# Optimization experiments

Measured on AMD Instinct MI355X. Metric: run time of the kernel, lower is better.

## Reference

```python
import jax, jax.numpy as jnp
import numpy as np

MAX_DEPTH = 83.0
PI = 3.1415926535
SCALE = 8
FOCAL = 715.0

def setup_inputs() -> dict:
    key = jax.random.key(0)
    ks = jax.random.split(key, 16)
    B, C, H, W = 16, 128, 44, 152
    x = jax.random.normal(ks[0], (B, C, H, W), dtype=jnp.float32)
    # reduction 1x1 convs: 128->64->32->16->8->4
    chans = [128, 64, 32, 16, 8, 4]
    inp = {"x": x}
    for i in range(5):
        cin, cout = chans[i], chans[i + 1]
        w = jax.random.normal(ks[1 + 2 * i], (cout, cin), dtype=jnp.float32) * (1.0 / np.sqrt(cin))
        b = jax.random.normal(ks[2 + 2 * i], (cout,), dtype=jnp.float32) * 0.01
        inp[f"w{i}"] = w
        inp[f"b{i}"] = b
    # final 1x1 conv: 4 -> 3
    inp["cw"] = jax.random.normal(ks[11], (3, 4), dtype=jnp.float32) * 0.5
    inp["cb"] = jax.random.normal(ks[12], (3,), dtype=jnp.float32) * 0.01
    return inp

def _lpg_block(x, w0, b0, w1, b1, w2, b2, w3, b3, w4, b4, cw, cb):
    # reduction chain: 1x1 conv + ELU
    for w, b in ((w0, b0), (w1, b1), (w2, b2), (w3, b3), (w4, b4)):
        x = jax.nn.elu(jnp.einsum('oc,bchw->bohw', w, x) + b[None, :, None, None])
    # 4 -> 3 conv producing (theta, phi, dist) logits
    y = jnp.einsum('oc,bchw->bohw', cw, x) + cb[None, :, None, None]
    theta = jax.nn.sigmoid(y[:, 0]) * PI / 6.0          # [B,H,W]
    phi = jax.nn.sigmoid(y[:, 1]) * PI * 2.0
    dist = jax.nn.sigmoid(y[:, 2]) * MAX_DEPTH
    n1 = jnp.sin(theta) * jnp.cos(phi)
    n2 = jnp.sin(theta) * jnp.sin(phi)
    n3 = jnp.cos(theta)
    n = jnp.stack([n1, n2, n3], axis=1)                  # [B,3,H,W]
    # F.normalize(p=2, dim=1, eps=1e-12)
    norm = jnp.sqrt(jnp.sum(n * n, axis=1, keepdims=True))
    n = n / jnp.maximum(norm, 1e-12)
    n1, n2, n3 = n[:, 0], n[:, 1], n[:, 2]
    # LPG expansion: depth[b, y*s+ii, x*s+jj] = dist / (n1*u[jj] + n2*v[ii] + n3)
    s = SCALE
    off = (jnp.arange(s, dtype=jnp.float32) - (s - 1) / 2.0) / s / FOCAL  # [s]
    v = off[:, None]   # rows (ii)
    u = off[None, :]   # cols (jj)
    denom = (n1[..., None, None] * u + n2[..., None, None] * v
             + n3[..., None, None])                       # [B,H,W,s,s]
    depth = dist[..., None, None] / denom                 # [B,H,W,s,s]
    B, H, W = dist.shape
    depth = jnp.transpose(depth, (0, 1, 3, 2, 4)).reshape(B, 1, H * s, W * s)
    return depth

def reference(x, w0, b0, w1, b1, w2, b2, w3, b3, w4, b4, cw, cb):
    return _lpg_block(x, w0, b0, w1, b1, w2, b2, w3, b3, w4, b4, cw, cb)
```

## Files before the change

kernel.cpp:

```cpp
#include <hip/hip_runtime.h>
#include <math.h>

#define HW_   6688
#define W_    152
#define NPIX  107008
#define OW_   1216
#define OHW_  428032

typedef _Float16 f16;
typedef _Float16 f16x2 __attribute__((ext_vector_type(2)));
typedef _Float16 f16x4 __attribute__((ext_vector_type(4)));
typedef _Float16 f16x8 __attribute__((ext_vector_type(8)));
typedef float    f32x4 __attribute__((ext_vector_type(4)));

#define MFMA(a,b,c) __builtin_amdgcn_mfma_f32_16x16x32_f16((a),(b),(c),0,0,0)

#define SX_STR   136
#define SA1_STR  40
#define SA2_OFF  5120
#define SA2_STR  24
#define SA3_OFF  8192
#define SA3_STR  16
#define SA0_OFFB 34816
#define SA0_STR  72
#define LDSB     53248

__device__ __forceinline__ float fast_sigmoid(float v) {
    return __builtin_amdgcn_rcpf(1.0f + __expf(-v));
}
__device__ __forceinline__ float eluf(float v) {
    return v > 0.0f ? v : (__expf(v) - 1.0f);
}
__device__ __forceinline__ void split8(const float* v, f16x8& hi, f16x8& lo) {
#pragma unroll
    for (int e = 0; e < 8; ++e) {
        f16 h = (f16)v[e];
        hi[e] = h;
        lo[e] = (f16)(v[e] - (float)h);
    }
}
__device__ __forceinline__ f16x4 elu_cvt4(f32x4 a) {
    f16x4 r;
    r[0] = (f16)eluf(a[0]); r[1] = (f16)eluf(a[1]);
    r[2] = (f16)eluf(a[2]); r[3] = (f16)eluf(a[3]);
    return r;
}

__global__ __launch_bounds__(256)
void lpg_mfma(const float* __restrict__ x,
              const float* __restrict__ w0, const float* __restrict__ b0,
              const float* __restrict__ w1, const float* __restrict__ b1,
              const float* __restrict__ w2, const float* __restrict__ b2,
              const float* __restrict__ w3, const float* __restrict__ b3,
              const float* __restrict__ w4, const float* __restrict__ b4,
              const float* __restrict__ cw, const float* __restrict__ cb,
              float* __restrict__ out) {
    __shared__ __align__(16) unsigned char S[LDSB];
    f16* SX  = (f16*)S;
    f16* SA0 = (f16*)(S + SA0_OFFB);

    const int tid  = threadIdx.x;
    const int wv   = __builtin_amdgcn_readfirstlane(tid >> 6);
    const int lane = tid & 63;
    const int p    = lane & 15;
    const int q    = lane >> 4;
    const int pixbase = blockIdx.x * 128;

    {
        const int i     = tid & 127;
        const int chalf = (tid >> 7) * 64;
        int pix = pixbase + i;
        int bb  = pix / HW_;
        int hw  = pix - bb * HW_;
        const float* xp = x + ((size_t)bb * 128 + chalf) * HW_ + hw;
        f16* dst = SX + i * SX_STR + chalf;
#pragma unroll 8
        for (int k = 0; k < 32; ++k) {
            float v0 = xp[(size_t)(2 * k) * HW_];
            float v1 = xp[(size_t)(2 * k + 1) * HW_];
            f16x2 h; h[0] = (f16)v0; h[1] = (f16)v1;
            *(f16x2*)(dst + 2 * k) = h;
        }
    }

    f16x8 w0h[4], w0l[4];
    {
        const float* wr = w0 + (wv * 16 + p) * 128 + q * 8;
#pragma unroll
        for (int kt = 0; kt < 4; ++kt) {
            float v[8];
#pragma unroll
            for (int e = 0; e < 8; ++e) v[e] = wr[kt * 32 + e];
            split8(v, w0h[kt], w0l[kt]);
        }
    }
    f16x8 w1h[2][2], w1l[2][2];
#pragma unroll
    for (int Mt = 0; Mt < 2; ++Mt)
#pragma unroll
        for (int kt = 0; kt < 2; ++kt) {
            float v[8];
#pragma unroll
            for (int e = 0; e < 8; ++e) v[e] = w1[(Mt * 16 + p) * 64 + kt * 32 + q * 8 + e];
            split8(v, w1h[Mt][kt], w1l[Mt][kt]);
        }
    f16x8 w2h, w2l;
    {
        float v[8];
#pragma unroll
        for (int e = 0; e < 8; ++e) v[e] = w2[p * 32 + q * 8 + e];
        split8(v, w2h, w2l);
    }
    f16x8 w3h, w3l;
    {
        float v[8];
        bool ok = (p < 8) && (q < 2);
#pragma unroll
        for (int e = 0; e < 8; ++e) v[e] = ok ? w3[p * 16 + q * 8 + e] : 0.0f;
        split8(v, w3h, w3l);
    }
    f16x8 w4h, w4l;
    {
        float v[8];
        bool ok = (p < 4) && (q == 0);
#pragma unroll
        for (int e = 0; e < 8; ++e) v[e] = ok ? w4[p * 8 + e] : 0.0f;
        split8(v, w4h, w4l);
    }
    f16x8 whh, whl;
    {
        float v[8];
        bool ok = (p < 3) && (q == 0);
#pragma unroll
        for (int e = 0; e < 8; ++e) v[e] = (ok && e < 4) ? cw[p * 4 + e] : 0.0f;
        split8(v, whh, whl);
    }

    const f32x4 z4 = {0.f, 0.f, 0.f, 0.f};
    f32x4 b0v  = *(const f32x4*)(b0 + wv * 16 + 4 * q);
    f32x4 b1v0 = *(const f32x4*)(b1 + 4 * q);
    f32x4 b1v1 = *(const f32x4*)(b1 + 16 + 4 * q);
    f32x4 b2v  = *(const f32x4*)(b2 + 4 * q);
    f32x4 b3v  = *(const f32x4*)(b3 + (q & 1) * 4);
    f32x4 b4v  = *(const f32x4*)(b4);
    float cb0v = cb[0], cb1v = cb[1], cb2v = cb[2];

    __syncthreads();

#pragma unroll 2
    for (int t = 0; t < 8; ++t) {
        const f16* bp = SX + (t * 16 + p) * SX_STR + q * 8;
        f32x4 acc = b0v;
#pragma unroll
        for (int kt = 0; kt < 4; ++kt) {
            f16x8 bf = *(const f16x8*)(bp + kt * 32);
            acc = MFMA(w0h[kt], bf, acc);
            acc = MFMA(w0l[kt], bf, acc);
        }
        *(f16x4*)(SA0 + (t * 16 + p) * SA0_STR + wv * 16 + 4 * q) = elu_cvt4(acc);
    }
    __syncthreads();

    const int i0a = wv * 32 + p;
    const int i0b = wv * 32 + 16 + p;

    {
        f32x4 cA0 = b1v0, cA1 = b1v1, cB0 = b1v0, cB1 = b1v1;
#pragma unroll
        for (int kt = 0; kt < 2; ++kt) {
            f16x8 bfA = *(const f16x8*)(SA0 + i0a * SA0_STR + kt * 32 + q * 8);
            f16x8 bfB = *(const f16x8*)(SA0 + i0b * SA0_STR + kt * 32 + q * 8);
            cA0 = MFMA(w1h[0][kt], bfA, cA0); cA0 = MFMA(w1l[0][kt], bfA, cA0);
            cA1 = MFMA(w1h[1][kt], bfA, cA1); cA1 = MFMA(w1l[1][kt], bfA, cA1);
            cB0 = MFMA(w1h[0][kt], bfB, cB0); cB0 = MFMA(w1l[0][kt], bfB, cB0);
            cB1 = MFMA(w1h[1][kt], bfB, cB1); cB1 = MFMA(w1l[1][kt], bfB, cB1);
        }
        *(f16x4*)(SX + i0a * SA1_STR + 4 * q)      = elu_cvt4(cA0);
        *(f16x4*)(SX + i0a * SA1_STR + 16 + 4 * q) = elu_cvt4(cA1);
        *(f16x4*)(SX + i0b * SA1_STR + 4 * q)      = elu_cvt4(cB0);
        *(f16x4*)(SX + i0b * SA1_STR + 16 + 4 * q) = elu_cvt4(cB1);
    }
    __syncthreads();

    {
        f16x8 bfA = *(const f16x8*)(SX + i0a * SA1_STR + q * 8);
        f16x8 bfB = *(const f16x8*)(SX + i0b * SA1_STR + q * 8);
        f32x4 cA = b2v, cB = b2v;
        cA = MFMA(w2h, bfA, cA); cA = MFMA(w2l, bfA, cA);
        cB = MFMA(w2h, bfB, cB); cB = MFMA(w2l, bfB, cB);
        *(f16x4*)(SX + SA2_OFF + i0a * SA2_STR + 4 * q) = elu_cvt4(cA);
        *(f16x4*)(SX + SA2_OFF + i0b * SA2_STR + 4 * q) = elu_cvt4(cB);
    }
    __syncthreads();

    {
        f16x8 bfA = *(const f16x8*)(SX + SA2_OFF + i0a * SA2_STR + (q & 1) * 8);
        f16x8 bfB = *(const f16x8*)(SX + SA2_OFF + i0b * SA2_STR + (q & 1) * 8);
        if (q >= 2) { bfA = (f16x8){}; bfB = (f16x8){}; }
        f32x4 cA = (q < 2) ? b3v : z4, cB = (q < 2) ? b3v : z4;
        cA = MFMA(w3h, bfA, cA); cA = MFMA(w3l, bfA, cA);
        cB = MFMA(w3h, bfB, cB); cB = MFMA(w3l, bfB, cB);
        if (q < 2) {
            *(f16x4*)(SX + SA3_OFF + i0a * SA3_STR + 4 * q) = elu_cvt4(cA);
            *(f16x4*)(SX + SA3_OFF + i0b * SA3_STR + 4 * q) = elu_cvt4(cB);
        }
    }
    __syncthreads();

    f32x4 cyA, cyB;
    {
        f16x8 bfA = *(const f16x8*)(SX + SA3_OFF + i0a * SA3_STR);
        f16x8 bfB = *(const f16x8*)(SX + SA3_OFF + i0b * SA3_STR);
        if (q != 0) { bfA = (f16x8){}; bfB = (f16x8){}; }
        f32x4 cA = (q == 0) ? b4v : z4, cB = (q == 0) ? b4v : z4;
        cA = MFMA(w4h, bfA, cA); cA = MFMA(w4l, bfA, cA);
        cB = MFMA(w4h, bfB, cB); cB = MFMA(w4l, bfB, cB);

        f16x8 hA = (f16x8){}, hB = (f16x8){};
        if (q == 0) {
#pragma unroll
            for (int e = 0; e < 4; ++e) {
                hA[e] = (f16)eluf(cA[e]);
                hB[e] = (f16)eluf(cB[e]);
            }
        }
        cyA = z4; cyB = z4;
        if (q == 0) {
            cyA[0] = cb0v; cyA[1] = cb1v; cyA[2] = cb2v;
            cyB[0] = cb0v; cyB[1] = cb1v; cyB[2] = cb2v;
        }
        cyA = MFMA(whh, hA, cyA); cyA = MFMA(whl, hA, cyA);
        cyB = MFMA(whh, hB, cyB); cyB = MFMA(whl, hB, cyB);
    }

#pragma unroll
    for (int nt = 0; nt < 2; ++nt) {
        const int i0 = wv * 32 + nt * 16 + p;
        float y0 = __shfl(nt ? cyB[0] : cyA[0], p);
        float y1 = __shfl(nt ? cyB[1] : cyA[1], p);
        float y2 = __shfl(nt ? cyB[2] : cyA[2], p);

        float theta = 0.5235987756f * fast_sigmoid(y0);
        float phi   = 6.2831853072f * fast_sigmoid(y1);
        float dist  = 83.0f         * fast_sigmoid(y2);
        float st = __sinf(theta), ct = __cosf(theta);
        float sp = __sinf(phi),   cp = __cosf(phi);
        float n1 = st * cp, n2 = st * sp, n3 = ct;
        float inv = __frsqrt_rn(fmaf(n1, n1, fmaf(n2, n2, n3 * n3)));
        n1 *= inv; n2 *= inv; n3 *= inv;

        const float ksc = 1.0f / (8.0f * 715.0f);
        float nu[8];
#pragma unroll
        for (int j = 0; j < 8; ++j) nu[j] = n1 * (((float)j - 3.5f) * ksc);

        int pix = pixbase + i0;
        int bb  = pix / HW_;
        int hw  = pix - bb * HW_;
        int hh  = hw / W_;
        int ww  = hw - hh * W_;
        const int obase = bb * OHW_ + (hh * 8) * OW_ + ww * 8;
#pragma unroll
        for (int r = 0; r < 2; ++r) {
            int i = q * 2 + r;
            float base = fmaf(n2, ((float)i - 3.5f) * ksc, n3);
            float4 r0, r1;
            r0.x = dist * __builtin_amdgcn_rcpf(base + nu[0]);
            r0.y = dist * __builtin_amdgcn_rcpf(base + nu[1]);
            r0.z = dist * __builtin_amdgcn_rcpf(base + nu[2]);
            r0.w = dist * __builtin_amdgcn_rcpf(base + nu[3]);
            r1.x = dist * __builtin_amdgcn_rcpf(base + nu[4]);
            r1.y = dist * __builtin_amdgcn_rcpf(base + nu[5]);
            r1.z = dist * __builtin_amdgcn_rcpf(base + nu[6]);
            r1.w = dist * __builtin_amdgcn_rcpf(base + nu[7]);
            float4* op = (float4*)(out + obase + i * OW_);
            op[0] = r0;
            op[1] = r1;
        }
    }
}

extern "C" void kernel_launch(void* const* d_in, const int* in_sizes, int n_in,
                              void* d_out, int out_size, void* d_ws, size_t ws_size,
                              hipStream_t stream) {
    const float* x  = (const float*)d_in[0];
    const float* w0 = (const float*)d_in[1];
    const float* b0 = (const float*)d_in[2];
    const float* w1 = (const float*)d_in[3];
    const float* b1 = (const float*)d_in[4];
    const float* w2 = (const float*)d_in[5];
    const float* b2 = (const float*)d_in[6];
    const float* w3 = (const float*)d_in[7];
    const float* b3 = (const float*)d_in[8];
    const float* w4 = (const float*)d_in[9];
    const float* b4 = (const float*)d_in[10];
    const float* cw = (const float*)d_in[11];
    const float* cb = (const float*)d_in[12];
    float* outp = (float*)d_out;

    lpg_mfma<<<NPIX / 128, 256, 0, stream>>>(x, w0, b0, w1, b1, w2, b2, w3, b3,
                                             w4, b4, cw, cb, outp);
}
```

Before: 34.05 us.

## Stage input channels in two halves to shrink LDS and raise occupancy

Layer 0's input is now staged into LDS in two 64-channel halves, with accumulators held across both passes. This cuts the shared buffer from about 52KB to about 38KB so more blocks can sit on a CU, and launch_bounds now asks for 4 blocks per SM. Later layers, where each wave touches only its own pixel rows, swap __syncthreads for a wave-level barrier. The cost is an extra block sync round, serialized global loads between the halves, and more accumulator registers held live (8 f32x4).

```diff
diff --git a/kernel.cpp b/kernel.cpp
--- a/kernel.cpp
+++ b/kernel.cpp
@@ -15,15 +15,15 @@
 
 #define MFMA(a,b,c) __builtin_amdgcn_mfma_f32_16x16x32_f16((a),(b),(c),0,0,0)
 
-#define SX_STR   136
+#define SXH_STR  72
 #define SA1_STR  40
 #define SA2_OFF  5120
 #define SA2_STR  24
 #define SA3_OFF  8192
 #define SA3_STR  16
-#define SA0_OFFB 34816
+#define SA0_OFF  10240
 #define SA0_STR  72
-#define LDSB     53248
+#define LDSF16   19456
 
 __device__ __forceinline__ float fast_sigmoid(float v) {
     return __builtin_amdgcn_rcpf(1.0f + __expf(-v));
@@ -45,8 +45,22 @@
     r[2] = (f16)eluf(a[2]); r[3] = (f16)eluf(a[3]);
     return r;
 }
-
-__global__ __launch_bounds__(256)
+__device__ __forceinline__ void wave_fence() {
+    __builtin_amdgcn_sched_barrier(0);
+    __builtin_amdgcn_wave_barrier();
+    __builtin_amdgcn_sched_barrier(0);
+}
+__device__ __forceinline__ void stage32(const float* __restrict__ xp, f16* dst) {
+#pragma unroll 8
+    for (int k = 0; k < 32; k += 2) {
+        float v0 = xp[(size_t)k * HW_];
+        float v1 = xp[(size_t)(k + 1) * HW_];
+        f16x2 h; h[0] = (f16)v0; h[1] = (f16)v1;
+        *(f16x2*)(dst + k) = h;
+    }
+}
+
+__global__ __launch_bounds__(256, 4)
 void lpg_mfma(const float* __restrict__ x,
               const float* __restrict__ w0, const float* __restrict__ b0,
               const float* __restrict__ w1, const float* __restrict__ b1,
@@ -55,9 +69,9 @@
               const float* __restrict__ w4, const float* __restrict__ b4,
               const float* __restrict__ cw, const float* __restrict__ cb,
               float* __restrict__ out) {
-    __shared__ __align__(16) unsigned char S[LDSB];
-    f16* SX  = (f16*)S;
-    f16* SA0 = (f16*)(S + SA0_OFFB);
+    __shared__ __align__(16) f16 S[LDSF16];
+    f16* SX  = S;
+    f16* SA0 = S + SA0_OFF;
 
     const int tid  = threadIdx.x;
     const int wv   = __builtin_amdgcn_readfirstlane(tid >> 6);
@@ -66,34 +80,64 @@
     const int q    = lane >> 4;
     const int pixbase = blockIdx.x * 128;
 
-    {
-        const int i     = tid & 127;
-        const int chalf = (tid >> 7) * 64;
-        int pix = pixbase + i;
-        int bb  = pix / HW_;
-        int hw  = pix - bb * HW_;
-        const float* xp = x + ((size_t)bb * 128 + chalf) * HW_ + hw;
-        f16* dst = SX + i * SX_STR + chalf;
-#pragma unroll 8
-        for (int k = 0; k < 32; ++k) {
-            float v0 = xp[(size_t)(2 * k) * HW_];
-            float v1 = xp[(size_t)(2 * k + 1) * HW_];
-            f16x2 h; h[0] = (f16)v0; h[1] = (f16)v1;
-            *(f16x2*)(dst + 2 * k) = h;
-        }
-    }
-
-    f16x8 w0h[4], w0l[4];
-    {
-        const float* wr = w0 + (wv * 16 + p) * 128 + q * 8;
-#pragma unroll
-        for (int kt = 0; kt < 4; ++kt) {
-            float v[8];
-#pragma unroll
-            for (int e = 0; e < 8; ++e) v[e] = wr[kt * 32 + e];
-            split8(v, w0h[kt], w0l[kt]);
-        }
-    }
+    const int i    = tid & 127;
+    const int csub = (tid >> 7) * 32;
+    int pixs = pixbase + i;
+    int bbs  = pixs / HW_;
+    int hws  = pixs - bbs * HW_;
+    const float* xps = x + ((size_t)bbs * 128 + csub) * HW_ + hws;
+    f16* dsts = SX + i * SXH_STR + csub;
+
+    stage32(xps, dsts);
+
+    const int w0row = (wv * 16 + p) * 128 + q * 8;
+    f16x8 w0h[2], w0l[2];
+#pragma unroll
+    for (int kt = 0; kt < 2; ++kt) {
+        float v[8];
+#pragma unroll
+        for (int e = 0; e < 8; ++e) v[e] = w0[w0row + kt * 32 + e];
+        split8(v, w0h[kt], w0l[kt]);
+    }
+    f32x4 acc[8];
+    {
+        f32x4 b0v = *(const f32x4*)(b0 + wv * 16 + 4 * q);
+#pragma unroll
+        for (int t = 0; t < 8; ++t) acc[t] = b0v;
+    }
+    __syncthreads();
+
+#pragma unroll 2
+    for (int t = 0; t < 8; ++t) {
+        const f16* bp = SX + (t * 16 + p) * SXH_STR + q * 8;
+        f16x8 bf0 = *(const f16x8*)(bp);
+        f16x8 bf1 = *(const f16x8*)(bp + 32);
+        acc[t] = MFMA(w0h[0], bf0, acc[t]); acc[t] = MFMA(w0l[0], bf0, acc[t]);
+        acc[t] = MFMA(w0h[1], bf1, acc[t]); acc[t] = MFMA(w0l[1], bf1, acc[t]);
+    }
+    __syncthreads();
+
+    stage32(xps + (size_t)64 * HW_, dsts);
+#pragma unroll
+    for (int kt = 0; kt < 2; ++kt) {
+        float v[8];
+#pragma unroll
+        for (int e = 0; e < 8; ++e) v[e] = w0[w0row + 64 + kt * 32 + e];
+        split8(v, w0h[kt], w0l[kt]);
+    }
+    __syncthreads();
+
+#pragma unroll 2
+    for (int t = 0; t < 8; ++t) {
+        const f16* bp = SX + (t * 16 + p) * SXH_STR + q * 8;
+        f16x8 bf0 = *(const f16x8*)(bp);
+        f16x8 bf1 = *(const f16x8*)(bp + 32);
+        acc[t] = MFMA(w0h[0], bf0, acc[t]); acc[t] = MFMA(w0l[0], bf0, acc[t]);
+        acc[t] = MFMA(w0h[1], bf1, acc[t]); acc[t] = MFMA(w0l[1], bf1, acc[t]);
+        *(f16x4*)(SA0 + (t * 16 + p) * SA0_STR + wv * 16 + 4 * q) = elu_cvt4(acc[t]);
+    }
+    __syncthreads();
+
     f16x8 w1h[2][2], w1l[2][2];
 #pragma unroll
     for (int Mt = 0; Mt < 2; ++Mt)
@@ -135,31 +179,13 @@
         for (int e = 0; e < 8; ++e) v[e] = (ok && e < 4) ? cw[p * 4 + e] : 0.0f;
         split8(v, whh, whl);
     }
-
     const f32x4 z4 = {0.f, 0.f, 0.f, 0.f};
-    f32x4 b0v  = *(const f32x4*)(b0 + wv * 16 + 4 * q);
     f32x4 b1v0 = *(const f32x4*)(b1 + 4 * q);
     f32x4 b1v1 = *(const f32x4*)(b1 + 16 + 4 * q);
     f32x4 b2v  = *(const f32x4*)(b2 + 4 * q);
     f32x4 b3v  = *(const f32x4*)(b3 + (q & 1) * 4);
     f32x4 b4v  = *(const f32x4*)(b4);
     float cb0v = cb[0], cb1v = cb[1], cb2v = cb[2];
-
-    __syncthreads();
-
-#pragma unroll 2
-    for (int t = 0; t < 8; ++t) {
-        const f16* bp = SX + (t * 16 + p) * SX_STR + q * 8;
-        f32x4 acc = b0v;
-#pragma unroll
-        for (int kt = 0; kt < 4; ++kt) {
-            f16x8 bf = *(const f16x8*)(bp + kt * 32);
-            acc = MFMA(w0h[kt], bf, acc);
-            acc = MFMA(w0l[kt], bf, acc);
-        }
-        *(f16x4*)(SA0 + (t * 16 + p) * SA0_STR + wv * 16 + 4 * q) = elu_cvt4(acc);
-    }
-    __syncthreads();
 
     const int i0a = wv * 32 + p;
     const int i0b = wv * 32 + 16 + p;
@@ -180,7 +206,7 @@
         *(f16x4*)(SX + i0b * SA1_STR + 4 * q)      = elu_cvt4(cB0);
         *(f16x4*)(SX + i0b * SA1_STR + 16 + 4 * q) = elu_cvt4(cB1);
     }
-    __syncthreads();
+    wave_fence();
 
     {
         f16x8 bfA = *(const f16x8*)(SX + i0a * SA1_STR + q * 8);
@@ -191,7 +217,7 @@
         *(f16x4*)(SX + SA2_OFF + i0a * SA2_STR + 4 * q) = elu_cvt4(cA);
         *(f16x4*)(SX + SA2_OFF + i0b * SA2_STR + 4 * q) = elu_cvt4(cB);
     }
-    __syncthreads();
+    wave_fence();
 
     {
         f16x8 bfA = *(const f16x8*)(SX + SA2_OFF + i0a * SA2_STR + (q & 1) * 8);
@@ -205,7 +231,7 @@
             *(f16x4*)(SX + SA3_OFF + i0b * SA3_STR + 4 * q) = elu_cvt4(cB);
         }
     }
-    __syncthreads();
+    wave_fence();
 
     f32x4 cyA, cyB;
     {
@@ -262,8 +288,8 @@
         const int obase = bb * OHW_ + (hh * 8) * OW_ + ww * 8;
 #pragma unroll
         for (int r = 0; r < 2; ++r) {
-            int i = q * 2 + r;
-            float base = fmaf(n2, ((float)i - 3.5f) * ksc, n3);
+            int irow = q * 2 + r;
+            float base = fmaf(n2, ((float)irow - 3.5f) * ksc, n3);
             float4 r0, r1;
             r0.x = dist * __builtin_amdgcn_rcpf(base + nu[0]);
             r0.y = dist * __builtin_amdgcn_rcpf(base + nu[1]);
@@ -273,7 +299,7 @@
             r1.y = dist * __builtin_amdgcn_rcpf(base + nu[5]);
             r1.z = dist * __builtin_amdgcn_rcpf(base + nu[6]);
             r1.w = dist * __builtin_amdgcn_rcpf(base + nu[7]);
-            float4* op = (float4*)(out + obase + i * OW_);
+            float4* op = (float4*)(out + obase + irow * OW_);
             op[0] = r0;
             op[1] = r1;
         }
```

After: 30.91 us. 9.2% less time.
